# Kernel optimization log

Hardware: AMD Instinct MI355X
Metric: run time of the kernel (lower is better)

The kernel has to match this reference:

```python
import jax, jax.numpy as jnp
from jax import lax
import numpy as np

D_IN = 512    # inputdim
HID = 128     # hiddendim
D_INNER = 2 * HID   # 256
D_PROJ = 2 * D_INNER  # 512
N_STATE = 16
R_DT = 8      # ceil(128/16)
B, H, W = 8, 32, 32


def _layernorm(y, g, b):
    mu = y.mean(-1, keepdims=True)
    var = ((y - mu) ** 2).mean(-1, keepdims=True)
    return (y - mu) / jnp.sqrt(var + 1e-5) * g + b


def _ssm(x, xw, dtw, dtb, Al, Dv, g, be):
    # x: [B, D, L] -> y: [B, L, D]  (Mamba selective scan, delta_softplus=True)
    Bb, D, L = x.shape
    n = Al.shape[1]
    xd = jnp.einsum('bdl,kd->blk', x, xw)             # [B,L,R+2N]
    dts = xd[..., :R_DT]
    Bs = xd[..., R_DT:R_DT + n]                        # [B,L,N]
    Cs = xd[..., R_DT + n:]                            # [B,L,N]
    delta = jax.nn.softplus(jnp.einsum('blr,dr->bld', dts, dtw) + dtb)  # [B,L,D]
    A = -jnp.exp(Al)                                   # [D,N]
    xt = x.transpose(0, 2, 1)                          # [B,L,D]
    dA = jnp.exp(delta[..., None] * A)                 # [B,L,D,N]
    dBx = delta[..., None] * Bs[:, :, None, :] * xt[..., None]  # [B,L,D,N]

    def step(h, inp):
        da, dbx, c = inp
        h = h * da + dbx
        return h, jnp.einsum('bdn,bn->bd', h, c)

    h0 = jnp.zeros((Bb, D, n), x.dtype)
    _, ys = lax.scan(step, h0, (dA.transpose(1, 0, 2, 3),
                                dBx.transpose(1, 0, 2, 3),
                                Cs.transpose(1, 0, 2)))
    y = ys.transpose(1, 0, 2) + xt * Dv                # [B,L,D]
    return _layernorm(y, g, be)


def _up2(y, h, w):
    Bb, L, C = y.shape
    img = y.transpose(0, 2, 1).reshape(Bb, C, h, w)
    img = jnp.repeat(jnp.repeat(img, 2, axis=2), 2, axis=3)
    return img.reshape(Bb, C, 4 * L).transpose(0, 2, 1)


def _conv1x1(x, w, b):
    return jnp.einsum('bchw,oc->bohw', x, w) + b[None, :, None, None]


def _conv2s2(x, w, b):
    out = lax.conv_general_dilated(x, w, (2, 2), 'VALID',
                                   dimension_numbers=('NCHW', 'OIHW', 'NCHW'))
    return out + b[None, :, None, None]


def _forward(input_f, in_w, in_b, c1_w, c1_b, c2_w, c2_b, c3_w, c3_b, out_w, out_b,
             xw1, dtw1, dtb1, Al1, Dv1, g1, be1,
             xw2, dtw2, dtb2, Al2, Dv2, g2, be2,
             xw3, dtw3, dtb3, Al3, Dv3, g3, be3):
    xz = _conv1x1(input_f, in_w, in_b)
    x, z = jnp.split(xz, 2, axis=1)
    f1 = _conv1x1(x, c1_w, c1_b)                      # [B,256,H,W]
    f2 = _conv2s2(f1, c2_w, c2_b)                     # [B,256,H/2,W/2]
    f3 = _conv2s2(f2, c3_w, c3_b)                     # [B,256,H/4,W/4]

    Bb, C, h3, w3 = f3.shape
    fx3 = f3.reshape(Bb, C, h3 * w3)
    y3 = _ssm(fx3, xw3, dtw3, dtb3, Al3, Dv3, g3, be3) + \
         jnp.flip(_ssm(jnp.flip(fx3, -1), xw3, dtw3, dtb3, Al3, Dv3, g3, be3), 1)
    y2_ = _up2(y3, h3, w3)

    _, _, h2, w2 = f2.shape
    fx2 = f2.reshape(Bb, C, h2 * w2)
    y2 = _ssm(fx2, xw2, dtw2, dtb2, Al2, Dv2, g2, be2) + \
         jnp.flip(_ssm(jnp.flip(fx2, -1), xw2, dtw2, dtb2, Al2, Dv2, g2, be2), 1) + y2_
    y1_ = _up2(y2, h2, w2)

    _, _, h1, w1 = f1.shape
    fx1 = f1.reshape(Bb, C, h1 * w1)
    # NOTE: source uses fssm1 forward and fssm2 on the flipped sequence
    y1 = _ssm(fx1, xw1, dtw1, dtb1, Al1, Dv1, g1, be1) + \
         jnp.flip(_ssm(jnp.flip(fx1, -1), xw2, dtw2, dtb2, Al2, Dv2, g2, be2), 1) + y1_

    out1 = y1.transpose(0, 2, 1).reshape(Bb, C, h1, w1)
    out = out1 * jax.nn.silu(z)
    return _conv1x1(out, out_w, out_b)


def setup_inputs() -> dict:
    key = jax.random.key(0)
    ks = iter(jax.random.split(key, 64))
    def nrm(shape, s=0.05):
        return (jax.random.normal(next(ks), shape, dtype=jnp.float32) * s)
    inp = {
        'input_f': jax.random.normal(next(ks), (B, D_IN, H, W), dtype=jnp.float32),
        'in_w': nrm((D_PROJ, D_IN)), 'in_b': nrm((D_PROJ,)),
        'c1_w': nrm((D_INNER, D_INNER)), 'c1_b': nrm((D_INNER,)),
        'c2_w': nrm((D_INNER, D_INNER, 2, 2)), 'c2_b': nrm((D_INNER,)),
        'c3_w': nrm((D_INNER, D_INNER, 2, 2)), 'c3_b': nrm((D_INNER,)),
        'out_w': nrm((D_IN, D_INNER)), 'out_b': nrm((D_IN,)),
    }
    Al = jnp.log(jnp.tile(jnp.arange(1, N_STATE + 1, dtype=jnp.float32), (D_INNER, 1)))
    for i in (1, 2, 3):
        inp[f'xw{i}'] = nrm((R_DT + 2 * N_STATE, D_INNER))
        inp[f'dtw{i}'] = nrm((D_INNER, R_DT), s=R_DT ** -0.5)
        inp[f'dtb{i}'] = nrm((D_INNER,)) - 4.0   # inv-softplus of small dt
        inp[f'Al{i}'] = Al
        inp[f'Dv{i}'] = jnp.ones((D_INNER,), jnp.float32)
        inp[f'g{i}'] = jnp.ones((D_INNER,), jnp.float32)
        inp[f'be{i}'] = jnp.zeros((D_INNER,), jnp.float32)
    return inp


def reference(input_f, in_w, in_b, c1_w, c1_b, c2_w, c2_b, c3_w, c3_b, out_w, out_b,
              xw1, dtw1, dtb1, Al1, Dv1, g1, be1,
              xw2, dtw2, dtb2, Al2, Dv2, g2, be2,
              xw3, dtw3, dtb3, Al3, Dv3, g3, be3):
    return _forward(input_f, in_w, in_b, c1_w, c1_b, c2_w, c2_b, c3_w, c3_b, out_w, out_b,
                    xw1, dtw1, dtb1, Al1, Dv1, g1, be1,
                    xw2, dtw2, dtb2, Al2, Dv2, g2, be2,
                    xw3, dtw3, dtb3, Al3, Dv3, g3, be3)
```

## Files before the change

### kernel.cpp

```cpp
#include <hip/hip_runtime.h>
#include <cstddef>

#define DEV static __device__ __forceinline__

typedef __attribute__((ext_vector_type(8))) short short8;
typedef __attribute__((ext_vector_type(4))) float floatx4;

DEV float siluf(float v) { return v / (1.f + expf(-v)); }

DEV unsigned short f2bf(float f) {
  unsigned int u = __float_as_uint(f);
  u += 0x7fff + ((u >> 16) & 1);
  return (unsigned short)(u >> 16);
}
DEV float bf2f(unsigned short u) {
  return __uint_as_float(((unsigned int)u) << 16);
}
DEV float4 bf2f4(ushort4 v) {
  return make_float4(bf2f(v.x), bf2f(v.y), bf2f(v.z), bf2f(v.w));
}

template <int CTRL>
DEV float qadd(float v) {
  int s = __builtin_amdgcn_update_dpp(__float_as_int(v), __float_as_int(v),
                                      CTRL, 0xF, 0xF, false);
  return v + __int_as_float(s);
}

__global__ __launch_bounds__(256) void prep_k(
    const float* __restrict__ in_w, const float* __restrict__ c1_w,
    const float* __restrict__ c2_w, const float* __restrict__ c3_w,
    const float* __restrict__ out_w, const float* __restrict__ xw1,
    const float* __restrict__ xw2, const float* __restrict__ xw3,
    unsigned short* __restrict__ wsW,
    const float* __restrict__ input_f, unsigned short* __restrict__ inT,
    const float* __restrict__ in_b, const float* __restrict__ c1_b,
    unsigned short* __restrict__ w_fz, float* __restrict__ bias_fz)
{
  __shared__ float tile[32][33];
  __shared__ float c1s[1024];
  __shared__ float part[32][8];
  int bid = blockIdx.x;
  int t = threadIdx.x;
  if (bid < 3960) {
    int gid = bid * 256 + t;
    float v;
    if      (gid < 262144)  v = in_w[gid];
    else if (gid < 327680)  v = c1_w[gid - 262144];
    else if (gid < 589824)  {
      int off = gid - 327680;
      int o = off >> 10, kk = off & 1023, ij = kk >> 8, c = kk & 255;
      v = c2_w[o * 1024 + c * 4 + ij];
    }
    else if (gid < 851968)  {
      int off = gid - 589824;
      int o = off >> 10, kk = off & 1023, ij = kk >> 8, c = kk & 255;
      v = c3_w[o * 1024 + c * 4 + ij];
    }
    else if (gid < 983040)  v = out_w[gid - 851968];
    else if (gid < 993280)  v = xw1[gid - 983040];
    else if (gid < 1003520) v = xw2[gid - 993280];
    else                    v = xw3[gid - 1003520];
    wsW[gid] = f2bf(v);
  } else if (bid < 8056) {
    int idx = bid - 3960;
    int b = idx >> 9, blk = idx & 511;
    int pt = blk & 31, ct = blk >> 5;
    int p0 = pt * 32, c0 = ct * 32;
    int r = t >> 5, cc = t & 31;
#pragma unroll
    for (int i = 0; i < 4; i++) {
      int row = r + 8 * i;
      tile[row][cc] = input_f[((size_t)b * 512 + c0 + row) * 1024 + p0 + cc];
    }
    __syncthreads();
#pragma unroll
    for (int i = 0; i < 4; i++) {
      int row = r + 8 * i;
      inT[((size_t)b * 1024 + p0 + row) * 512 + c0 + cc] = f2bf(tile[cc][row]);
    }
  } else if (bid < 8184) {
    int ib = bid - 8056;
    int ot = ib >> 1;
    int ci = ((ib & 1) << 8) + t;
#pragma unroll
    for (int rr = 0; rr < 4; rr++)
      c1s[rr * 256 + t] = c1_w[(size_t)(ot * 4 + rr) * 256 + t];
    __syncthreads();
    float acc[4] = {0.f, 0.f, 0.f, 0.f};
#pragma unroll 4
    for (int m = 0; m < 256; m++) {
      float wv = in_w[(size_t)m * 512 + ci];
#pragma unroll
      for (int rr = 0; rr < 4; rr++) acc[rr] += c1s[rr * 256 + m] * wv;
    }
#pragma unroll
    for (int rr = 0; rr < 4; rr++)
      w_fz[(size_t)(ot * 4 + rr) * 512 + ci] = f2bf(acc[rr]);
  } else if (bid < 8192) {
    int jb = bid - 8184;
    int oo = t >> 3, mc = t & 7;
    int o = jb * 32 + oo;
    float s = 0.f;
#pragma unroll 8
    for (int mm = 0; mm < 32; mm++) {
      int m = mc * 32 + mm;
      s += c1_w[(size_t)o * 256 + m] * in_b[m];
    }
    part[oo][mc] = s;
    __syncthreads();
    if (mc == 0) {
      float a = c1_b[o];
#pragma unroll
      for (int k = 0; k < 8; k++) a += part[oo][k];
      bias_fz[o] = a;
    }
    if (jb == 0) bias_fz[256 + t] = in_b[256 + t];
  } else {
    int r = bid - 8192;
    const float* src = in_w + (size_t)(256 + r) * 512;
    w_fz[(size_t)(256 + r) * 512 + t]       = f2bf(src[t]);
    w_fz[(size_t)(256 + r) * 512 + 256 + t] = f2bf(src[256 + t]);
  }
}

template <int EPI>
DEV void mgemm_body(const unsigned short* __restrict__ A, long long sA,
                    const unsigned short* __restrict__ B, long long sB,
                    const float* __restrict__ bias,
                    void* __restrict__ O1, void* __restrict__ O2,
                    void* __restrict__ O3,
                    int M, int N, int K, int Mt, int Nt, int bid)
{
  __shared__ __align__(16) unsigned short Ab[2 * 128 * 40];
  __shared__ __align__(16) unsigned short Bb[2 * 128 * 40];
  int tiles = Mt * Nt;
  int bb = bid / tiles;
  int rr = bid - bb * tiles;
  int m0 = (rr / Nt) * 128;
  int n0 = (rr % Nt) * 128;
  const unsigned short* Ap = A + (size_t)bb * sA;
  const unsigned short* Bp = B + (size_t)bb * sB;

  int t = threadIdx.x;
  int lane = t & 63;
  int wm = ((t >> 7) & 1) * 64;
  int wn = ((t >> 6) & 1) * 64;
  int l15 = lane & 15, quad = lane >> 4;

  int srow = t >> 1;
  int shalf = (t & 1) * 16;
  int arow = m0 + srow; if (arow > M - 1) arow = M - 1;
  int brow = n0 + srow; if (brow > N - 1) brow = N - 1;
  const unsigned short* ap = Ap + (size_t)arow * K + shalf;
  const unsigned short* bp = Bp + (size_t)brow * K + shalf;
  unsigned short* as = &Ab[srow * 40 + shalf];
  unsigned short* bs = &Bb[srow * 40 + shalf];

  floatx4 acc[4][4] = {};

  uint4 a0 = *(const uint4*)(ap);
  uint4 a1 = *(const uint4*)(ap + 8);
  uint4 b0 = *(const uint4*)(bp);
  uint4 b1 = *(const uint4*)(bp + 8);
  *(uint4*)as = a0; *(uint4*)(as + 8) = a1;
  *(uint4*)bs = b0; *(uint4*)(bs + 8) = b1;
  __syncthreads();
  int cur = 0;
  for (int k0 = 0; k0 < K; k0 += 32) {
    bool last = (k0 + 32 >= K);
    if (!last) {
      a0 = *(const uint4*)(ap + k0 + 32);
      a1 = *(const uint4*)(ap + k0 + 40);
      b0 = *(const uint4*)(bp + k0 + 32);
      b1 = *(const uint4*)(bp + k0 + 40);
    }
    int co = cur * 5120;
    short8 af[4], bfr[4];
#pragma unroll
    for (int i = 0; i < 4; i++)
      af[i] = *(const short8*)&Ab[co + (wm + i * 16 + l15) * 40 + quad * 8];
#pragma unroll
    for (int j = 0; j < 4; j++)
      bfr[j] = *(const short8*)&Bb[co + (wn + j * 16 + l15) * 40 + quad * 8];
#pragma unroll
    for (int i = 0; i < 4; i++)
#pragma unroll
      for (int j = 0; j < 4; j++)
        acc[i][j] = __builtin_amdgcn_mfma_f32_16x16x32_bf16(af[i], bfr[j],
                                                            acc[i][j], 0, 0, 0);
    if (!last) {
      int no = 5120 - co;
      *(uint4*)(as + no) = a0; *(uint4*)(as + no + 8) = a1;
      *(uint4*)(bs + no) = b0; *(uint4*)(bs + no + 8) = b1;
      __syncthreads();
      cur ^= 1;
    }
  }

  if (EPI == 1) {
    unsigned short* F1t = (unsigned short*)O1;
    unsigned short* F1b = (unsigned short*)O2;
    unsigned short* Sz  = (unsigned short*)O3;
    float bn[4]; int nn[4];
#pragma unroll
    for (int j = 0; j < 4; j++) { nn[j] = n0 + wn + j * 16 + l15; bn[j] = bias[nn[j]]; }
#pragma unroll
    for (int i = 0; i < 4; i++) {
      int pixb = m0 + wm + i * 16 + quad * 4;
#pragma unroll
      for (int j = 0; j < 4; j++) {
        int n = nn[j];
        float vr[4];
#pragma unroll
        for (int r = 0; r < 4; r++) vr[r] = acc[i][j][r] + bn[j];
        if (n < 256) {
#pragma unroll
          for (int r = 0; r < 4; r++)
            F1t[((size_t)bb * 1024 + pixb + r) * 256 + n] = f2bf(vr[r]);
          ushort4 o4;
          o4.x = f2bf(vr[0]); o4.y = f2bf(vr[1]); o4.z = f2bf(vr[2]); o4.w = f2bf(vr[3]);
          *(ushort4*)&F1b[((size_t)bb * 256 + n) * 1024 + pixb] = o4;
        } else {
#pragma unroll
          for (int r = 0; r < 4; r++)
            Sz[((size_t)bb * 1024 + pixb + r) * 256 + (n - 256)] =
                f2bf(siluf(vr[r]));
        }
      }
    }
  } else {
#pragma unroll
    for (int i = 0; i < 4; i++) {
      int m = m0 + wm + i * 16 + quad * 4;
#pragma unroll
      for (int j = 0; j < 4; j++) {
        int n = n0 + wn + j * 16 + l15;
        if (m < M && n < N) {
          float vr[4];
#pragma unroll
          for (int r = 0; r < 4; r++)
            vr[r] = acc[i][j][r] + (bias ? bias[m + r] : 0.f);
          float* Y0 = (float*)O1;
          float* yp = &Y0[((size_t)bb * M + m) * N + n];
#pragma unroll
          for (int r = 0; r < 4; r++) yp[(size_t)r * N] = vr[r];
        }
      }
    }
  }
}

template <int EPI>
__global__ __launch_bounds__(256) void mgemm_k(
    const unsigned short* __restrict__ A, long long sA,
    const unsigned short* __restrict__ B, long long sB,
    const float* __restrict__ bias, void* __restrict__ O1, void* __restrict__ O2,
    void* __restrict__ O3,
    int M, int N, int K, int Mt, int Nt)
{
  mgemm_body<EPI>(A, sA, B, sB, bias, O1, O2, O3, M, N, K, Mt, Nt, blockIdx.x);
}

__global__ __launch_bounds__(256) void cgemm_k(
    const unsigned short* __restrict__ A,
    const unsigned short* __restrict__ B, long long sB,
    const float* __restrict__ bias,
    unsigned short* __restrict__ O1, unsigned short* __restrict__ O2,
    int M, int N, int K, int Mt, int Nt)
{
  __shared__ __align__(16) unsigned short Ab[2][64 * 72];
  __shared__ __align__(16) unsigned short Bb[2][32 * 72];
  int bid = blockIdx.x;
  int tiles = Mt * Nt;
  int bb = bid / tiles;
  int rr = bid - bb * tiles;
  int m0 = (rr / Nt) * 64;
  int n0 = (rr % Nt) * 32;
  const unsigned short* Bp = B + (size_t)bb * sB;

  int t = threadIdx.x, lane = t & 63;
  int wm = ((t >> 7) & 1) * 32;
  int wn = ((t >> 6) & 1) * 16;
  int l15 = lane & 15, quad = lane >> 4;

  int ar = t >> 2, ac = (t & 3) * 16;
  int brc = (t >> 2) & 31, bc = (t & 3) * 16;
  const unsigned short* apc = A + (size_t)(m0 + ar) * K + ac;
  const unsigned short* bpc = Bp + (size_t)(n0 + brc) * K + bc;

  floatx4 acc2[2] = {};

  uint4 av0 = *(const uint4*)(apc);
  uint4 av1 = *(const uint4*)(apc + 8);
  uint4 bv0 = {}, bv1 = {};
  if (t < 128) { bv0 = *(const uint4*)(bpc); bv1 = *(const uint4*)(bpc + 8); }
  {
    unsigned short* asc = &Ab[0][0] + ar * 72 + ac;
    *(uint4*)asc = av0; *(uint4*)(asc + 8) = av1;
    if (t < 128) {
      unsigned short* bsc = &Bb[0][0] + brc * 72 + bc;
      *(uint4*)bsc = bv0; *(uint4*)(bsc + 8) = bv1;
    }
  }
  __syncthreads();
  int cur = 0;
  for (int k0 = 0; k0 < K; k0 += 64) {
    bool last = (k0 + 64 >= K);
    if (!last) {
      av0 = *(const uint4*)(apc + k0 + 64);
      av1 = *(const uint4*)(apc + k0 + 72);
      if (t < 128) {
        bv0 = *(const uint4*)(bpc + k0 + 64);
        bv1 = *(const uint4*)(bpc + k0 + 72);
      }
    }
    const unsigned short* Ac = &Ab[cur][0];
    const unsigned short* Bc = &Bb[cur][0];
    short8 afc[2][2], bfc[2];
#pragma unroll
    for (int i = 0; i < 2; i++)
#pragma unroll
      for (int kk = 0; kk < 2; kk++)
        afc[i][kk] = *(const short8*)&Ac[(wm + i * 16 + l15) * 72 + kk * 32 + quad * 8];
#pragma unroll
    for (int kk = 0; kk < 2; kk++)
      bfc[kk] = *(const short8*)&Bc[(wn + l15) * 72 + kk * 32 + quad * 8];
#pragma unroll
    for (int kk = 0; kk < 2; kk++) {
      acc2[0] = __builtin_amdgcn_mfma_f32_16x16x32_bf16(afc[0][kk], bfc[kk], acc2[0], 0, 0, 0);
      acc2[1] = __builtin_amdgcn_mfma_f32_16x16x32_bf16(afc[1][kk], bfc[kk], acc2[1], 0, 0, 0);
    }
    if (!last) {
      unsigned short* asn = &Ab[cur ^ 1][0] + ar * 72 + ac;
      *(uint4*)asn = av0; *(uint4*)(asn + 8) = av1;
      if (t < 128) {
        unsigned short* bsn = &Bb[cur ^ 1][0] + brc * 72 + bc;
        *(uint4*)bsn = bv0; *(uint4*)(bsn + 8) = bv1;
      }
      __syncthreads();
      cur ^= 1;
    }
  }

#pragma unroll
  for (int i = 0; i < 2; i++) {
    int m = m0 + wm + i * 16 + quad * 4;
    int n = n0 + wn + l15;
    float vr[4];
#pragma unroll
    for (int r = 0; r < 4; r++) vr[r] = acc2[i][r] + bias[m + r];
#pragma unroll
    for (int r = 0; r < 4; r++)
      O1[((size_t)bb * M + m + r) * N + n] = f2bf(vr[r]);
    ushort4 o;
    o.x = f2bf(vr[0]); o.y = f2bf(vr[1]); o.z = f2bf(vr[2]); o.w = f2bf(vr[3]);
    *(ushort4*)&O2[((size_t)bb * N + n) * M + m] = o;
  }
}

__global__ __launch_bounds__(256) void fat1_k(
    const unsigned short* __restrict__ w_xw12, const unsigned short* __restrict__ f1t,
    float* __restrict__ xd12, unsigned short* __restrict__ ic2)
{
  int bid = blockIdx.x;
  if (bid < 64) {
    mgemm_body<0>(w_xw12, 0, f1t, 1024 * 256, nullptr, xd12, nullptr, nullptr,
                  80, 1024, 256, 1, 8, bid);
  } else {
    int idx = (bid - 64) * 256 + threadIdx.x;
    int cs = idx & 31, ij = (idx >> 5) & 3, n = (idx >> 7) & 255, b = idx >> 15;
    int i = ij >> 1, j = ij & 1;
    int y = n >> 4, x = n & 15;
    int pix = (2 * y + i) * 32 + 2 * x + j;
    uint4 v = *(const uint4*)&f1t[((size_t)b * 1024 + pix) * 256 + cs * 8];
    *(uint4*)&ic2[((size_t)b * 256 + n) * 1024 + ij * 256 + cs * 8] = v;
  }
}

__global__ __launch_bounds__(256) void fat2_k(
    const unsigned short* __restrict__ w_xw2, const unsigned short* __restrict__ f2t,
    float* __restrict__ xd2, unsigned short* __restrict__ ic3)
{
  int bid = blockIdx.x;
  if (bid < 16) {
    mgemm_body<0>(w_xw2, 0, f2t, 256 * 256, nullptr, xd2, nullptr, nullptr,
                  40, 256, 256, 1, 2, bid);
  } else {
    int idx = (bid - 16) * 256 + threadIdx.x;
    int cs = idx & 31, ij = (idx >> 5) & 3, n = (idx >> 7) & 63, b = idx >> 13;
    int i = ij >> 1, j = ij & 1;
    int y = n >> 3, x = n & 7;
    int pix = (2 * y + i) * 16 + 2 * x + j;
    uint4 v = *(const uint4*)&f2t[((size_t)b * 256 + pix) * 256 + cs * 8];
    *(uint4*)&ic3[((size_t)b * 64 + n) * 1024 + ij * 256 + cs * 8] = v;
  }
}

__global__ __launch_bounds__(256) void post_all_k(
    const float* __restrict__ xd12, const float* __restrict__ xd2,
    const float* __restrict__ xd3,
    const float* __restrict__ dtw1, const float* __restrict__ dtb1,
    const float* __restrict__ dtw2, const float* __restrict__ dtb2,
    const float* __restrict__ dtw3, const float* __restrict__ dtb3,
    float* __restrict__ d1f, float* __restrict__ bc1f,
    float* __restrict__ d1b, float* __restrict__ bc1b,
    float* __restrict__ d2g, float* __restrict__ bc2,
    float* __restrict__ d3g, float* __restrict__ bc3)
{
  int bid = blockIdx.x;
  const float* xd; int bstride, L; const float *dtw, *dtb; float *dg, *bg;
  int lt, b;
  if (bid < 512) {
    int r = bid; lt = r & 63; b = r >> 6;
    xd = xd12; bstride = 80 * 1024; L = 1024; dtw = dtw1; dtb = dtb1; dg = d1f; bg = bc1f;
  } else if (bid < 1024) {
    int r = bid - 512; lt = r & 63; b = r >> 6;
    xd = xd12 + 40 * 1024; bstride = 80 * 1024; L = 1024; dtw = dtw2; dtb = dtb2; dg = d1b; bg = bc1b;
  } else if (bid < 1152) {
    int r = bid - 1024; lt = r & 15; b = r >> 4;
    xd = xd2; bstride = 40 * 256; L = 256; dtw = dtw2; dtb = dtb2; dg = d2g; bg = bc2;
  } else {
    int r = bid - 1152; lt = r & 3; b = r >> 2;
    xd = xd3; bstride = 40 * 64; L = 64; dtw = dtw3; dtb = dtb3; dg = d3g; bg = bc3;
  }
  int l0 = lt * 16;
  __shared__ float dl[8][16];
  int t = threadIdx.x;
  const float* xb = xd + (size_t)b * bstride + l0;
  if (t < 128) {
    int r = t >> 4, l = t & 15;
    dl[r][l] = xb[(size_t)r * L + l];
  } else {
    int tt = t - 128;
    int c = tt >> 2, seg = tt & 3;
    float4 v = *(const float4*)&xb[(size_t)(8 + c) * L + seg * 4];
    *(float4*)&bg[((size_t)b * 32 + c) * L + l0 + seg * 4] = v;
  }
  __syncthreads();
  int d = t;
  float dtwv[8];
#pragma unroll
  for (int r = 0; r < 8; r++) dtwv[r] = dtw[d * 8 + r];
  float dtbv = dtb[d];
  float spv[16];
#pragma unroll
  for (int l = 0; l < 16; l++) {
    float s = dtbv;
#pragma unroll
    for (int r = 0; r < 8; r++) s += dl[r][l] * dtwv[r];
    spv[l] = fmaxf(s, 0.f) + log1pf(expf(-fabsf(s)));
  }
  float* dout = dg + ((size_t)b * 256 + d) * L + l0;
#pragma unroll
  for (int i = 0; i < 4; i++)
    *(float4*)&dout[4 * i] = make_float4(spv[4 * i], spv[4 * i + 1],
                                         spv[4 * i + 2], spv[4 * i + 3]);
}

#define SCAN_STEPA(DVV, DXV, BVV) {                     \
    float e_ = __builtin_amdgcn_exp2f((DVV) * A2);      \
    h = h * e_ + (BVV) * (DXV);                         \
    S += (DVV); }

__global__ __launch_bounds__(256) void scanA_k(
    const unsigned short* __restrict__ f1b, const unsigned short* __restrict__ f2b,
    const unsigned short* __restrict__ f3b,
    const float* __restrict__ d1f, const float* __restrict__ bc1f,
    const float* __restrict__ d1b, const float* __restrict__ bc1b,
    const float* __restrict__ d2,  const float* __restrict__ bc2,
    const float* __restrict__ d3,  const float* __restrict__ bc3,
    const float* __restrict__ Al1, const float* __restrict__ Al2,
    const float* __restrict__ Al3,
    float* __restrict__ cP, float* __restrict__ cQ)
{
  __shared__ __align__(16) float lds[48][36];
  int bid = blockIdx.x;
  int sid, tseg, L; const unsigned short* xin; const float *dlp, *bcp, *Alp;
  if (bid < 8192) {
    sid = bid >> 5; tseg = bid & 31; L = 1024; xin = f1b;
    if (((sid >> 4) & 1) == 0) { dlp = d1f; bcp = bc1f; Alp = Al1; }
    else                       { dlp = d1b; bcp = bc1b; Alp = Al2; }
  } else if (bid < 10240) {
    int idx = bid - 8192; sid = idx >> 3; tseg = idx & 7; L = 256;
    xin = f2b; dlp = d2; bcp = bc2; Alp = Al2;
  } else {
    int idx = bid - 10240; sid = idx >> 1; tseg = idx & 1; L = 64;
    xin = f3b; dlp = d3; bcp = bc3; Alp = Al3;
  }
  int b = sid >> 5, dir = (sid >> 4) & 1, g = sid & 15;
  int t = threadIdx.x, n = t & 15, dloc = t >> 4, d = g * 16 + dloc;
  int mbase = dir ? (L - 32 * (tseg + 1)) : 32 * tseg;

  if (t < 128) {
    int r0 = t >> 3, cs = t & 7;
    const float* p0 = dlp + ((size_t)b * 256 + g * 16 + r0) * L + mbase;
    const unsigned short* p1 = xin + ((size_t)b * 256 + g * 16 + r0) * L + mbase;
    float4 v0 = *(const float4*)(p0 + cs * 4);
    float4 xf = bf2f4(*(const ushort4*)(p1 + cs * 4));
    float4 dx = make_float4(v0.x * xf.x, v0.y * xf.y, v0.z * xf.z, v0.w * xf.w);
    *(float4*)&lds[r0][cs * 4]      = v0;
    *(float4*)&lds[16 + r0][cs * 4] = dx;
  } else {
    int r0 = (t - 128) >> 3, cs = t & 7;
    const float* p2 = bcp + ((size_t)b * 32 + r0) * L + mbase;
    float4 v2 = *(const float4*)(p2 + cs * 4);
    *(float4*)&lds[32 + r0][cs * 4] = v2;
  }
  __syncthreads();

  float A2 = -expf(Alp[d * 16 + n]) * 1.442695040888963f;
  float h = 0.f, S = 0.f;
  if (dir == 0) {
#pragma unroll
    for (int g4 = 0; g4 < 8; g4++) {
      int cb = 4 * g4;
      float4 dv4 = *(const float4*)&lds[dloc][cb];
      float4 dx4 = *(const float4*)&lds[16 + dloc][cb];
      float4 bv4 = *(const float4*)&lds[32 + n][cb];
      SCAN_STEPA(dv4.x, dx4.x, bv4.x);
      SCAN_STEPA(dv4.y, dx4.y, bv4.y);
      SCAN_STEPA(dv4.z, dx4.z, bv4.z);
      SCAN_STEPA(dv4.w, dx4.w, bv4.w);
    }
  } else {
#pragma unroll
    for (int g4 = 0; g4 < 8; g4++) {
      int cb = 28 - 4 * g4;
      float4 dv4 = *(const float4*)&lds[dloc][cb];
      float4 dx4 = *(const float4*)&lds[16 + dloc][cb];
      float4 bv4 = *(const float4*)&lds[32 + n][cb];
      SCAN_STEPA(dv4.w, dx4.w, bv4.w);
      SCAN_STEPA(dv4.z, dx4.z, bv4.z);
      SCAN_STEPA(dv4.y, dx4.y, bv4.y);
      SCAN_STEPA(dv4.x, dx4.x, bv4.x);
    }
  }
  cP[(size_t)bid * 256 + t] = __builtin_amdgcn_exp2f(S * A2);
  cQ[(size_t)bid * 256 + t] = h;
}

#define QSTEP(DS, XU, CI, II) {                                         \
    float4 bv = *(const float4*)&ld_b[CI][n0];                          \
    float4 cv = *(const float4*)&ld_c[CI][n0];                          \
    float xs_ = bf2f(XU) * (DS);                                        \
    float4 e_;                                                          \
    e_.x = __builtin_amdgcn_exp2f((DS) * A4.x);                         \
    e_.y = __builtin_amdgcn_exp2f((DS) * A4.y);                         \
    e_.z = __builtin_amdgcn_exp2f((DS) * A4.z);                         \
    e_.w = __builtin_amdgcn_exp2f((DS) * A4.w);                         \
    h4.x = h4.x * e_.x + bv.x * xs_;                                    \
    h4.y = h4.y * e_.y + bv.y * xs_;                                    \
    h4.z = h4.z * e_.z + bv.z * xs_;                                    \
    h4.w = h4.w * e_.w + bv.w * xs_;                                    \
    float pp_ = h4.x * cv.x + h4.y * cv.y + h4.z * cv.z + h4.w * cv.w;  \
    pp_ = qadd<0xB1>(pp_);                                              \
    pp_ = qadd<0x4E>(pp_);                                              \
    ysel = (nq == (II)) ? pp_ : ysel; }

DEV float4 pcomb(float4 P, float4 h, float4 Q) {
  return make_float4(P.x * h.x + Q.x, P.y * h.y + Q.y,
                     P.z * h.z + Q.z, P.w * h.w + Q.w);
}

__global__ __launch_bounds__(256) void scanC_k(
    const unsigned short* __restrict__ f1b, const unsigned short* __restrict__ f2b,
    const unsigned short* __restrict__ f3b,
    const float* __restrict__ d1f, const float* __restrict__ bc1f,
    const float* __restrict__ d1b, const float* __restrict__ bc1b,
    const float* __restrict__ d2,  const float* __restrict__ bc2,
    const float* __restrict__ d3,  const float* __restrict__ bc3,
    float* __restrict__ y1f, float* __restrict__ y1b,
    float* __restrict__ y2f, float* __restrict__ y2b,
    float* __restrict__ y3f, float* __restrict__ y3b,
    const float* __restrict__ Al1, const float* __restrict__ Dv1,
    const float* __restrict__ Al2, const float* __restrict__ Dv2,
    const float* __restrict__ Al3, const float* __restrict__ Dv3,
    const float* __restrict__ cP, const float* __restrict__ cQ)
{
  __shared__ __align__(16) float ld_d[64][36];
  __shared__ __align__(16) unsigned short ld_xs[64][40];
  __shared__ __align__(16) float ld_b[32][20];
  __shared__ __align__(16) float ld_c[32][20];

  int bid = blockIdx.x;
  int b, dir, g4, tseg, L, lvl;
  const unsigned short* xin; const float *dlp, *bcp, *Alp, *Dvp; float* yo;
  if (bid < 2048) {
    b = bid >> 8; dir = (bid >> 7) & 1; g4 = (bid >> 5) & 3; tseg = bid & 31;
    L = 1024; xin = f1b; lvl = 1;
    if (dir == 0) { dlp = d1f; bcp = bc1f; Alp = Al1; Dvp = Dv1; yo = y1f; }
    else          { dlp = d1b; bcp = bc1b; Alp = Al2; Dvp = Dv2; yo = y1b; }
  } else if (bid < 2560) {
    int idx = bid - 2048;
    b = idx >> 6; dir = (idx >> 5) & 1; g4 = (idx >> 3) & 3; tseg = idx & 7;
    L = 256; xin = f2b; lvl = 2;
    dlp = d2; bcp = bc2; Alp = Al2; Dvp = Dv2; yo = dir ? y2b : y2f;
  } else {
    int idx = bid - 2560;
    b = idx >> 4; dir = (idx >> 3) & 1; g4 = (idx >> 1) & 3; tseg = idx & 1;
    L = 64; xin = f3b; lvl = 3;
    dlp = d3; bcp = bc3; Alp = Al3; Dvp = Dv3; yo = dir ? y3b : y3f;
  }
  int mbase = dir ? (L - 32 * (tseg + 1)) : 32 * tseg;
  int t = threadIdx.x;
  int dl = t >> 2, nq = t & 3, n0 = nq * 4;
  int d = g4 * 64 + dl;

  {
    int rr = t >> 2, q = t & 3;
    const float* dr = dlp + ((size_t)b * 256 + g4 * 64 + rr) * L + mbase;
    const unsigned short* xr = xin + ((size_t)b * 256 + g4 * 64 + rr) * L + mbase;
#pragma unroll
    for (int j = 0; j < 2; ++j) {
      int c = q * 4 + 16 * j;
      float4 dv = *(const float4*)(dr + c);
      ushort4 xu = *(const ushort4*)(xr + c);
      *(float4*)&ld_d[rr][c] = dv;
      *(ushort4*)&ld_xs[rr][c] = xu;
    }
    if (t < 128) {
      int nn = t >> 3, c4 = t & 7;
      const float* br = bcp + ((size_t)b * 32 + nn) * L + mbase + c4 * 4;
      float4 bv = *(const float4*)br;
      ld_b[c4 * 4 + 0][nn] = bv.x; ld_b[c4 * 4 + 1][nn] = bv.y;
      ld_b[c4 * 4 + 2][nn] = bv.z; ld_b[c4 * 4 + 3][nn] = bv.w;
    } else {
      int tt = t - 128;
      int nn = tt >> 3, c4 = tt & 7;
      const float* cr = bcp + ((size_t)b * 32 + 16 + nn) * L + mbase + c4 * 4;
      float4 cv = *(const float4*)cr;
      ld_c[c4 * 4 + 0][nn] = cv.x; ld_c[c4 * 4 + 1][nn] = cv.y;
      ld_c[c4 * 4 + 2][nn] = cv.z; ld_c[c4 * 4 + 3][nn] = cv.w;
    }
  }

  float4 A4;
  A4.x = -expf(Alp[d * 16 + n0 + 0]) * 1.442695040888963f;
  A4.y = -expf(Alp[d * 16 + n0 + 1]) * 1.442695040888963f;
  A4.z = -expf(Alp[d * 16 + n0 + 2]) * 1.442695040888963f;
  A4.w = -expf(Alp[d * 16 + n0 + 3]) * 1.442695040888963f;
  float Dvv = Dvp[d];

  float4 h4 = make_float4(0.f, 0.f, 0.f, 0.f);
  if (tseg > 0) {
    int gold = g4 * 4 + (dl >> 4);
    int soff = (lvl == 1) ? (b * 32 + dir * 16 + gold) * 32
             : (lvl == 2) ? 8192 + (b * 32 + dir * 16 + gold) * 8
                          : 10240 + (b * 32 + dir * 16 + gold) * 2;
    size_t cbase = (size_t)soff * 256 + (size_t)((dl & 15) * 16 + n0);
    int s = 0;
    for (; s + 4 <= tseg; s += 4) {
      const float* p = &cP[cbase + (size_t)s * 256];
      const float* q = &cQ[cbase + (size_t)s * 256];
      float4 P0 = *(const float4*)(p);       float4 Q0 = *(const float4*)(q);
      float4 P1 = *(const float4*)(p + 256); float4 Q1 = *(const float4*)(q + 256);
      float4 P2 = *(const float4*)(p + 512); float4 Q2 = *(const float4*)(q + 512);
      float4 P3 = *(const float4*)(p + 768); float4 Q3 = *(const float4*)(q + 768);
      h4 = pcomb(P0, h4, Q0); h4 = pcomb(P1, h4, Q1);
      h4 = pcomb(P2, h4, Q2); h4 = pcomb(P3, h4, Q3);
    }
    for (; s < tseg; ++s) {
      float4 P = *(const float4*)&cP[cbase + (size_t)s * 256];
      float4 Q = *(const float4*)&cQ[cbase + (size_t)s * 256];
      h4 = pcomb(P, h4, Q);
    }
  }
  __syncthreads();

  float* ybase = yo + ((size_t)b * L + mbase) * 256 + d;
  if (dir == 0) {
#pragma unroll
    for (int p = 0; p < 2; ++p) {
      float yk[4];
#pragma unroll
      for (int j = 0; j < 4; ++j) {
        int cb = 16 * p + 4 * j;
        float4 dv4 = *(const float4*)&ld_d[dl][cb];
        ushort4 xu4 = *(const ushort4*)&ld_xs[dl][cb];
        float ysel = 0.f;
        QSTEP(dv4.x, xu4.x, cb + 0, 0);
        QSTEP(dv4.y, xu4.y, cb + 1, 1);
        QSTEP(dv4.z, xu4.z, cb + 2, 2);
        QSTEP(dv4.w, xu4.w, cb + 3, 3);
        yk[j] = ysel;
      }
#pragma unroll
      for (int j = 0; j < 4; ++j) {
        int cst = 16 * p + 4 * j + nq;
        float xv = bf2f(ld_xs[dl][cst]);
        ybase[(size_t)cst * 256] = yk[j] + xv * Dvv;
      }
    }
  } else {
#pragma unroll
    for (int p = 0; p < 2; ++p) {
      float yk[4];
#pragma unroll
      for (int j = 0; j < 4; ++j) {
        int cb = 28 - 16 * p - 4 * j;
        float4 dv4 = *(const float4*)&ld_d[dl][cb];
        ushort4 xu4 = *(const ushort4*)&ld_xs[dl][cb];
        float ysel = 0.f;
        QSTEP(dv4.w, xu4.w, cb + 3, 0);
        QSTEP(dv4.z, xu4.z, cb + 2, 1);
        QSTEP(dv4.y, xu4.y, cb + 1, 2);
        QSTEP(dv4.x, xu4.x, cb + 0, 3);
        yk[j] = ysel;
      }
#pragma unroll
      for (int j = 0; j < 4; ++j) {
        int cst = 28 - 16 * p - 4 * j + (3 - nq);
        float xv = bf2f(ld_xs[dl][cst]);
        ybase[(size_t)cst * 256] = yk[j] + xv * Dvv;
      }
    }
  }
}

template <int OUTBF>
__global__ __launch_bounds__(256) void ln_combine(
    const float* __restrict__ yf, const float* __restrict__ yb,
    const float* __restrict__ gf, const float* __restrict__ bef,
    const float* __restrict__ gb, const float* __restrict__ beb,
    const float* __restrict__ up, int Wc,
    const unsigned short* __restrict__ szb, void* __restrict__ outv,
    int L, int Lsh, int Wfsh)
{
  int t = threadIdx.x;
  int row = blockIdx.x * 4 + (t >> 6);
  int lane = t & 63;
  int b = row >> Lsh, l = row & (L - 1);
  size_t base = (size_t)row * 256 + lane * 4;
  float4 vf = *(const float4*)&yf[base];
  float4 vb = *(const float4*)&yb[base];
  float4 s;
  s.x = vf.x + vf.y + vf.z + vf.w;
  s.y = vf.x * vf.x + vf.y * vf.y + vf.z * vf.z + vf.w * vf.w;
  s.z = vb.x + vb.y + vb.z + vb.w;
  s.w = vb.x * vb.x + vb.y * vb.y + vb.z * vb.z + vb.w * vb.w;
#pragma unroll
  for (int m = 1; m < 64; m <<= 1) {
    s.x += __shfl_xor(s.x, m);
    s.y += __shfl_xor(s.y, m);
    s.z += __shfl_xor(s.z, m);
    s.w += __shfl_xor(s.w, m);
  }
  const float inv = 1.f / 256.f;
  float muf = s.x * inv, varf = s.y * inv - muf * muf;
  float mub = s.z * inv, varb = s.w * inv - mub * mub;
  float rf = rsqrtf(varf + 1e-5f);
  float rb = rsqrtf(varb + 1e-5f);
  int dc = lane * 4;
  float4 gfv = *(const float4*)&gf[dc];
  float4 befv = *(const float4*)&bef[dc];
  float4 gbv = *(const float4*)&gb[dc];
  float4 bebv = *(const float4*)&beb[dc];
  float4 v;
  v.x = (vf.x - muf) * rf * gfv.x + befv.x + (vb.x - mub) * rb * gbv.x + bebv.x;
  v.y = (vf.y - muf) * rf * gfv.y + befv.y + (vb.y - mub) * rb * gbv.y + bebv.y;
  v.z = (vf.z - muf) * rf * gfv.z + befv.z + (vb.z - mub) * rb * gbv.z + bebv.z;
  v.w = (vf.w - muf) * rf * gfv.w + befv.w + (vb.w - mub) * rb * gbv.w + bebv.w;
  if (up) {
    int y = l >> Wfsh, x = l & ((1 << Wfsh) - 1);
    int lc = (y >> 1) * Wc + (x >> 1);
    float4 uv = *(const float4*)&up[((size_t)b * (L >> 2) + lc) * 256 + dc];
    v.x += uv.x; v.y += uv.y; v.z += uv.z; v.w += uv.w;
  }
  if (szb) {
    ushort4 su = *(const ushort4*)&szb[base];
    v.x *= bf2f(su.x); v.y *= bf2f(su.y); v.z *= bf2f(su.z); v.w *= bf2f(su.w);
  }
  if (OUTBF) {
    ushort4 o;
    o.x = f2bf(v.x); o.y = f2bf(v.y); o.z = f2bf(v.z); o.w = f2bf(v.w);
    *(ushort4*)&((unsigned short*)outv)[base] = o;
  } else {
    *(float4*)&((float*)outv)[base] = v;
  }
}

extern "C" void kernel_launch(void* const* d_in, const int* in_sizes, int n_in,
                              void* d_out, int out_size, void* d_ws, size_t ws_size,
                              hipStream_t stream) {
  (void)in_sizes; (void)n_in; (void)out_size; (void)ws_size;
  const float* input_f = (const float*)d_in[0];
  const float* in_w  = (const float*)d_in[1];
  const float* in_b  = (const float*)d_in[2];
  const float* c1_w  = (const float*)d_in[3];
  const float* c1_b  = (const float*)d_in[4];
  const float* c2_w  = (const float*)d_in[5];
  const float* c2_b  = (const float*)d_in[6];
  const float* c3_w  = (const float*)d_in[7];
  const float* c3_b  = (const float*)d_in[8];
  const float* out_w = (const float*)d_in[9];
  const float* out_b = (const float*)d_in[10];
  const float* xw1  = (const float*)d_in[11];
  const float* dtw1 = (const float*)d_in[12];
  const float* dtb1 = (const float*)d_in[13];
  const float* Al1  = (const float*)d_in[14];
  const float* Dv1  = (const float*)d_in[15];
  const float* g1   = (const float*)d_in[16];
  const float* be1  = (const float*)d_in[17];
  const float* xw2  = (const float*)d_in[18];
  const float* dtw2 = (const float*)d_in[19];
  const float* dtb2 = (const float*)d_in[20];
  const float* Al2  = (const float*)d_in[21];
  const float* Dv2  = (const float*)d_in[22];
  const float* g2   = (const float*)d_in[23];
  const float* be2  = (const float*)d_in[24];
  const float* xw3  = (const float*)d_in[25];
  const float* dtw3 = (const float*)d_in[26];
  const float* dtb3 = (const float*)d_in[27];
  const float* Al3  = (const float*)d_in[28];
  const float* Dv3  = (const float*)d_in[29];
  const float* g3   = (const float*)d_in[30];
  const float* be3  = (const float*)d_in[31];

  float* ws = (float*)d_ws;
  constexpr size_t M1 = 2097152;
  float* d1f = ws;
  unsigned short* f1t = (unsigned short*)(ws + M1);
  float* y1f = ws + M1;
  unsigned short* szb = (unsigned short*)(ws + 2 * M1);
  unsigned short* f1b = (unsigned short*)(ws + 3 * M1);
  unsigned short* G = (unsigned short*)(ws + 3 * M1) + 2097152;
  float* d1b = ws + 4 * M1;
  unsigned short* inT = (unsigned short*)(ws + 5 * M1);
  unsigned short* ic2 = inT;
  unsigned short* ic3 = inT + 2097152;
  float* y1b = ws + 5 * M1;
  size_t o = 6 * M1;
  unsigned short* f2b = (unsigned short*)(ws + o); o += 524288;
  unsigned short* f3b = (unsigned short*)(ws + o); o += 131072;
  float* bc1f = ws + o; o += 262144;
  float* bc1b = ws + o; o += 262144;
  float* d2   = ws + o; o += 524288;
  float* bc2  = ws + o; o += 65536;
  float* d3   = ws + o; o += 131072;
  float* bc3  = ws + o; o += 16384;
  float* y2f  = ws + o; o += 524288;
  float* y2b  = ws + o; o += 524288;
  float* y3f  = ws + o; o += 131072;
  float* y3b  = ws + o; o += 131072;
  float* y3c  = ws + o; o += 131072;
  float* y2c  = ws + o; o += 524288;
  float* cP   = ws + o; o += 2752512;
  float* cQ   = ws + o; o += 2752512;
  unsigned short* wsW = (unsigned short*)(ws + o); o += 506880;
  float* bias_fz = ws + o; o += 512;
  unsigned short* w_fz = (unsigned short*)(ws + o); o += 131072;
  float* xd12 = cP;
  float* xd2  = cP + 655360;
  float* xd3  = cP + 737280;
  unsigned short* f2t = (unsigned short*)cQ;
  unsigned short* f3t = (unsigned short*)(cQ + 262144);
  unsigned short* w_c2   = wsW + 327680;
  unsigned short* w_c3   = wsW + 589824;
  unsigned short* w_out  = wsW + 851968;
  unsigned short* w_xw12 = wsW + 983040;
  unsigned short* w_xw2  = wsW + 993280;
  unsigned short* w_xw3  = wsW + 1003520;

  dim3 blk(256);

  prep_k<<<dim3(8448), blk, 0, stream>>>(in_w, c1_w, c2_w, c3_w, out_w,
                                         xw1, xw2, xw3, wsW, input_f, inT,
                                         in_b, c1_b, w_fz, bias_fz);
  mgemm_k<1><<<dim3(256), blk, 0, stream>>>(inT, 1024 * 512, w_fz, 0, bias_fz,
                                            f1t, f1b, szb, 1024, 512, 512, 8, 4);
  fat1_k<<<dim3(1088), blk, 0, stream>>>(w_xw12, f1t, xd12, ic2);
  cgemm_k<<<dim3(256), blk, 0, stream>>>(w_c2, ic2, 256 * 1024, c2_b,
                                         f2b, f2t, 256, 256, 1024, 4, 8);
  fat2_k<<<dim3(272), blk, 0, stream>>>(w_xw2, f2t, xd2, ic3);
  cgemm_k<<<dim3(64), blk, 0, stream>>>(w_c3, ic3, 64 * 1024, c3_b,
                                        f3b, f3t, 256, 64, 1024, 4, 2);
  mgemm_k<0><<<dim3(8), blk, 0, stream>>>(w_xw3, 0, f3t, 64 * 256, nullptr,
                                          xd3, nullptr, nullptr, 40, 64, 256, 1, 1);
  post_all_k<<<dim3(1184), blk, 0, stream>>>(xd12, xd2, xd3,
                                             dtw1, dtb1, dtw2, dtb2, dtw3, dtb3,
                                             d1f, bc1f, d1b, bc1b, d2, bc2, d3, bc3);
  scanA_k<<<dim3(10752), blk, 0, stream>>>(f1b, f2b, f3b,
                                           d1f, bc1f, d1b, bc1b, d2, bc2, d3, bc3,
                                           Al1, Al2, Al3, cP, cQ);
  scanC_k<<<dim3(2688), blk, 0, stream>>>(f1b, f2b, f3b,
                                          d1f, bc1f, d1b, bc1b, d2, bc2, d3, bc3,
                                          y1f, y1b, y2f, y2b, y3f, y3b,
                                          Al1, Dv1, Al2, Dv2, Al3, Dv3, cP, cQ);
  ln_combine<0><<<dim3(128), blk, 0, stream>>>(y3f, y3b, g3, be3, g3, be3,
                                               nullptr, 0, nullptr, y3c, 64, 6, 3);
  ln_combine<0><<<dim3(512), blk, 0, stream>>>(y2f, y2b, g2, be2, g2, be2,
                                               y3c, 8, nullptr, y2c, 256, 8, 4);
  ln_combine<1><<<dim3(2048), blk, 0, stream>>>(y1f, y1b, g1, be1, g2, be2,
                                                y2c, 16, szb, G, 1024, 10, 5);
  mgemm_k<0><<<dim3(256), blk, 0, stream>>>(w_out, 0, G, 1024 * 256, out_b,
                                            (float*)d_out, nullptr, nullptr,
                                            512, 1024, 256, 4, 8);
}
```

Measured before the change: 332.0 us.

## Add chunk-carry scan kernel so scan consumers load one precomputed state

Adds a scanB kernel that serially combines the per-chunk (P,Q) decay and state pairs into each chunk's starting hidden state cH. scanC now reads that single state instead of folding up to 31 earlier chunks per block. This removes redundant, quadratic-in-segments carry work and cP/cQ traffic from scanC. In exchange it adds a kernel launch, a serial 32-step pass, and a larger workspace buffer.

After: 325.1 us. -2.1%, faster.

```diff
diff --git a/kernel.cpp b/kernel.cpp
--- a/kernel.cpp
+++ b/kernel.cpp
@@ -538,6 +538,23 @@
   }
   cP[(size_t)bid * 256 + t] = __builtin_amdgcn_exp2f(S * A2);
   cQ[(size_t)bid * 256 + t] = h;
+}
+
+__global__ __launch_bounds__(256) void scanB_k(
+    const float* __restrict__ cP, const float* __restrict__ cQ,
+    float* __restrict__ cH)
+{
+  int bid = blockIdx.x, t = threadIdx.x;
+  int base, S;
+  if (bid < 256)      { base = bid * 32; S = 32; }
+  else if (bid < 512) { base = 8192 + (bid - 256) * 8; S = 8; }
+  else                { base = 10240 + (bid - 512) * 2; S = 2; }
+  float h = 0.f;
+  for (int s = 0; s < S; ++s) {
+    size_t off = (size_t)(base + s) * 256 + t;
+    cH[off] = h;
+    h = cP[off] * h + cQ[off];
+  }
 }
 
 #define QSTEP(DS, XU, CI, II) {                                         \
@@ -558,11 +575,6 @@
     pp_ = qadd<0x4E>(pp_);                                              \
     ysel = (nq == (II)) ? pp_ : ysel; }
 
-DEV float4 pcomb(float4 P, float4 h, float4 Q) {
-  return make_float4(P.x * h.x + Q.x, P.y * h.y + Q.y,
-                     P.z * h.z + Q.z, P.w * h.w + Q.w);
-}
-
 __global__ __launch_bounds__(256) void scanC_k(
     const unsigned short* __restrict__ f1b, const unsigned short* __restrict__ f2b,
     const unsigned short* __restrict__ f3b,
@@ -576,7 +588,7 @@
     const float* __restrict__ Al1, const float* __restrict__ Dv1,
     const float* __restrict__ Al2, const float* __restrict__ Dv2,
     const float* __restrict__ Al3, const float* __restrict__ Dv3,
-    const float* __restrict__ cP, const float* __restrict__ cQ)
+    const float* __restrict__ cH)
 {
   __shared__ __align__(16) float ld_d[64][36];
   __shared__ __align__(16) unsigned short ld_xs[64][40];
@@ -607,6 +619,16 @@
   int dl = t >> 2, nq = t & 3, n0 = nq * 4;
   int d = g4 * 64 + dl;
 
+  float4 h4;
+  {
+    int gold = g4 * 4 + (dl >> 4);
+    int soff = (lvl == 1) ? (b * 32 + dir * 16 + gold) * 32
+             : (lvl == 2) ? 8192 + (b * 32 + dir * 16 + gold) * 8
+                          : 10240 + (b * 32 + dir * 16 + gold) * 2;
+    h4 = *(const float4*)&cH[(size_t)(soff + tseg) * 256 +
+                             (size_t)((dl & 15) * 16 + n0)];
+  }
+
   {
     int rr = t >> 2, q = t & 3;
     const float* dr = dlp + ((size_t)b * 256 + g4 * 64 + rr) * L + mbase;
@@ -641,31 +663,6 @@
   A4.z = -expf(Alp[d * 16 + n0 + 2]) * 1.442695040888963f;
   A4.w = -expf(Alp[d * 16 + n0 + 3]) * 1.442695040888963f;
   float Dvv = Dvp[d];
-
-  float4 h4 = make_float4(0.f, 0.f, 0.f, 0.f);
-  if (tseg > 0) {
-    int gold = g4 * 4 + (dl >> 4);
-    int soff = (lvl == 1) ? (b * 32 + dir * 16 + gold) * 32
-             : (lvl == 2) ? 8192 + (b * 32 + dir * 16 + gold) * 8
-                          : 10240 + (b * 32 + dir * 16 + gold) * 2;
-    size_t cbase = (size_t)soff * 256 + (size_t)((dl & 15) * 16 + n0);
-    int s = 0;
-    for (; s + 4 <= tseg; s += 4) {
-      const float* p = &cP[cbase + (size_t)s * 256];
-      const float* q = &cQ[cbase + (size_t)s * 256];
-      float4 P0 = *(const float4*)(p);       float4 Q0 = *(const float4*)(q);
-      float4 P1 = *(const float4*)(p + 256); float4 Q1 = *(const float4*)(q + 256);
-      float4 P2 = *(const float4*)(p + 512); float4 Q2 = *(const float4*)(q + 512);
-      float4 P3 = *(const float4*)(p + 768); float4 Q3 = *(const float4*)(q + 768);
-      h4 = pcomb(P0, h4, Q0); h4 = pcomb(P1, h4, Q1);
-      h4 = pcomb(P2, h4, Q2); h4 = pcomb(P3, h4, Q3);
-    }
-    for (; s < tseg; ++s) {
-      float4 P = *(const float4*)&cP[cbase + (size_t)s * 256];
-      float4 Q = *(const float4*)&cQ[cbase + (size_t)s * 256];
-      h4 = pcomb(P, h4, Q);
-    }
-  }
   __syncthreads();
 
   float* ybase = yo + ((size_t)b * L + mbase) * 256 + d;
@@ -847,6 +844,7 @@
   float* y2c  = ws + o; o += 524288;
   float* cP   = ws + o; o += 2752512;
   float* cQ   = ws + o; o += 2752512;
+  float* cH   = ws + o; o += 2752512;
   unsigned short* wsW = (unsigned short*)(ws + o); o += 506880;
   float* bias_fz = ws + o; o += 512;
   unsigned short* w_fz = (unsigned short*)(ws + o); o += 131072;
@@ -883,10 +881,11 @@
   scanA_k<<<dim3(10752), blk, 0, stream>>>(f1b, f2b, f3b,
                                            d1f, bc1f, d1b, bc1b, d2, bc2, d3, bc3,
                                            Al1, Al2, Al3, cP, cQ);
+  scanB_k<<<dim3(768), blk, 0, stream>>>(cP, cQ, cH);
   scanC_k<<<dim3(2688), blk, 0, stream>>>(f1b, f2b, f3b,
                                           d1f, bc1f, d1b, bc1b, d2, bc2, d3, bc3,
                                           y1f, y1b, y2f, y2b, y3f, y3b,
-                                          Al1, Dv1, Al2, Dv2, Al3, Dv3, cP, cQ);
+                                          Al1, Dv1, Al2, Dv2, Al3, Dv3, cH);
   ln_combine<0><<<dim3(128), blk, 0, stream>>>(y3f, y3b, g3, be3, g3, be3,
                                                nullptr, 0, nullptr, y3c, 64, 6, 3);
   ln_combine<0><<<dim3(512), blk, 0, stream>>>(y2f, y2b, g2, be2, g2, be2,
```
